# Kernel tuning notes

Measured on AMD Instinct MI355X. Metric: run time of the kernel, lower is better.

## Reference

```python
import jax, jax.numpy as jnp
import numpy as np

N = 50000
E = 800000
D_IN = 64
D_E = 32
H = 128
EPS = 1e-5


def _seg_mean(msgs, dst, n):
    s = jax.ops.segment_sum(msgs, dst, num_segments=n)
    c = jax.ops.segment_sum(jnp.ones((dst.shape[0], 1), msgs.dtype), dst, num_segments=n)
    return s / jnp.maximum(c, 1.0)


def _bn(h, g, b, m, v):
    return g * (h - m) * jax.lax.rsqrt(v + EPS) + b


def setup_inputs() -> dict:
    key = jax.random.key(0)
    ks = jax.random.split(key, 32)
    inp = {
        "x": jax.random.normal(ks[0], (N, D_IN), jnp.float32),
        "edge_index_0": jax.random.randint(ks[1], (2, E), 0, N),
        "edge_index_1": jax.random.randint(ks[2], (2, E), 0, N),
        "edge_index_2": jax.random.randint(ks[3], (2, E), 0, N),
        "edge_attr_0": jax.random.normal(ks[4], (E, D_E), jnp.float32),
        # conv1: Linear(D_IN + D_E -> H)
        "W1": jax.random.normal(ks[5], (H, D_IN + D_E), jnp.float32) * 0.1,
        "b1": jnp.zeros((H,), jnp.float32),
        "g1": jnp.ones((H,), jnp.float32), "be1": jnp.zeros((H,), jnp.float32),
        "m1": jax.random.normal(ks[6], (H,), jnp.float32) * 0.1,
        "v1": jax.random.uniform(ks[7], (H,), jnp.float32) + 0.5,
        # SAGEConv2: lin_l (bias) on aggregated neighbors + lin_r (no bias) on self
        "Wl2": jax.random.normal(ks[8], (H, H), jnp.float32) * 0.1,
        "bl2": jnp.zeros((H,), jnp.float32),
        "Wr2": jax.random.normal(ks[9], (H, H), jnp.float32) * 0.1,
        "g2": jnp.ones((H,), jnp.float32), "be2": jnp.zeros((H,), jnp.float32),
        "m2": jax.random.normal(ks[10], (H,), jnp.float32) * 0.1,
        "v2": jax.random.uniform(ks[11], (H,), jnp.float32) + 0.5,
        # SAGEConv3
        "Wl3": jax.random.normal(ks[12], (H, H), jnp.float32) * 0.1,
        "bl3": jnp.zeros((H,), jnp.float32),
        "Wr3": jax.random.normal(ks[13], (H, H), jnp.float32) * 0.1,
        "g3": jnp.ones((H,), jnp.float32), "be3": jnp.zeros((H,), jnp.float32),
        "m3": jax.random.normal(ks[14], (H,), jnp.float32) * 0.1,
        "v3": jax.random.uniform(ks[15], (H,), jnp.float32) + 0.5,
        # mlp: Linear(H + D_IN -> 64) -> ReLU -> Linear(64 -> 1)
        "W4": jax.random.normal(ks[16], (64, H + D_IN), jnp.float32) * 0.1,
        "b4": jnp.zeros((64,), jnp.float32),
        "W5": jax.random.normal(ks[17], (1, 64), jnp.float32) * 0.1,
        "b5": jnp.zeros((1,), jnp.float32),
    }
    return inp


def reference(x, edge_index_0, edge_index_1, edge_index_2, edge_attr_0,
              W1, b1, g1, be1, m1, v1,
              Wl2, bl2, Wr2, g2, be2, m2, v2,
              Wl3, bl3, Wr3, g3, be3, m3, v3,
              W4, b4, W5, b5):
    n = x.shape[0]
    init = x
    # conv1: gather x_j + edge_attr, concat, linear, mean scatter, relu (update)
    msg = jnp.concatenate([x[edge_index_0[0]], edge_attr_0], axis=-1) @ W1.T + b1  # [E,H]
    h = jax.nn.relu(_seg_mean(msg, edge_index_0[1], n))
    h = jax.nn.relu(_bn(h, g1, be1, m1, v1))  # dropout: eval (identity)
    # conv2: SAGEConv = lin_l(mean_j x_j) + lin_r(x)
    agg = _seg_mean(h[edge_index_1[0]], edge_index_1[1], n)
    h = agg @ Wl2.T + bl2 + h @ Wr2.T
    h = jax.nn.relu(_bn(h, g2, be2, m2, v2))
    # conv3
    agg = _seg_mean(h[edge_index_2[0]], edge_index_2[1], n)
    h = agg @ Wl3.T + bl3 + h @ Wr3.T
    h = jax.nn.relu(_bn(h, g3, be3, m3, v3))
    # readout mlp on [h, initial_embedding]
    z = jnp.concatenate([h, init], axis=1)
    z = jax.nn.relu(z @ W4.T + b4)
    out = (z @ W5.T + b5).squeeze(-1)  # [N]
    return out
```

## Files before the change

kernel.cpp:

```cpp
#include <hip/hip_runtime.h>
#include <hip/hip_bf16.h>
#include <stdint.h>

#define NN 50000
#define NE 800000
#define EPS 1e-5f

#define KB 196
#define SH 8
#define NPB 256
#define RCAP 4500
#define PTP 512
#define PT2 2048

typedef __attribute__((ext_vector_type(8))) short bf16x8;
typedef __attribute__((ext_vector_type(4))) float floatx4;

static __device__ __forceinline__ float bf2f(unsigned int u){
  union { unsigned int i; float f; } c; c.i = u << 16; return c.f;
}
static __device__ __forceinline__ unsigned short f2bf(float f){
  union { float f; unsigned int i; } c; c.f = f;
  unsigned int x = c.i;
  return (unsigned short)((x + 0x7fffu + ((x >> 16) & 1u)) >> 16);
}

#define CVT_X   3200000
#define CVT_W1  3212288
#define CVT_WL2 3228672
#define CVT_WR2 3245056
#define CVT_WL3 3261440
#define CVT_WR3 3277824
#define CVT_END 3290112
__global__ void k_cvt_all(const float* __restrict__ x,  const float* __restrict__ W1,
                          const float* __restrict__ Wl2, const float* __restrict__ Wr2,
                          const float* __restrict__ Wl3, const float* __restrict__ Wr3,
                          const float* __restrict__ W4,
                          unsigned short* __restrict__ xb,  unsigned short* __restrict__ W1b,
                          unsigned short* __restrict__ Wl2b, unsigned short* __restrict__ Wr2b,
                          unsigned short* __restrict__ Wl3b, unsigned short* __restrict__ Wr3b,
                          unsigned short* __restrict__ W4b, int* __restrict__ gcur){
  int i = blockIdx.x * 256 + threadIdx.x;
  if(i >= CVT_END) return;
  if(i < 3 * KB) gcur[i] = 0;
  if(i < CVT_X)        xb[i] = f2bf(x[i]);
  else if(i < CVT_W1)  W1b[i - CVT_X]    = f2bf(W1[i - CVT_X]);
  else if(i < CVT_WL2) Wl2b[i - CVT_W1]  = f2bf(Wl2[i - CVT_W1]);
  else if(i < CVT_WR2) Wr2b[i - CVT_WL2] = f2bf(Wr2[i - CVT_WL2]);
  else if(i < CVT_WL3) Wl3b[i - CVT_WR2] = f2bf(Wl3[i - CVT_WR2]);
  else if(i < CVT_WR3) Wr3b[i - CVT_WL3] = f2bf(Wr3[i - CVT_WL3]);
  else                 W4b[i - CVT_WR3]  = f2bf(W4[i - CVT_WR3]);
}

__global__ void k_partP(const int* __restrict__ ei, const float* __restrict__ ea,
                        int* __restrict__ gcur,
                        int2* __restrict__ recDS, unsigned int* __restrict__ recEA){
  __shared__ int2 stage[PTP];
  __shared__ int slotArr[PTP];
  __shared__ unsigned int pay[PTP * 16];
  __shared__ int hist[KB], ex[KB], cur[KB], gbase[KB];
  __shared__ int tot;
  int tid = threadIdx.x;
  int tile = blockIdx.x * PTP;
  int cnt_local = NE - tile; if(cnt_local > PTP) cnt_local = PTP;
  for(int i = tid; i < KB; i += 256) hist[i] = 0;
  __syncthreads();
  int dst[2], src[2];
  #pragma unroll
  for(int j = 0; j < 2; j++){
    int t = j * 256 + tid;
    if(t < cnt_local){ src[j] = ei[tile + t]; dst[j] = ei[NE + tile + t]; atomicAdd(&hist[dst[j] >> SH], 1); }
    else dst[j] = -1;
  }
  __syncthreads();
  if(tid == 0){ int run = 0; for(int b = 0; b < KB; b++){ ex[b] = run; cur[b] = run; run += hist[b]; } tot = run; }
  if(tid < KB) gbase[tid] = atomicAdd(&gcur[tid], hist[tid]);
  __syncthreads();
  #pragma unroll
  for(int j = 0; j < 2; j++){
    if(dst[j] >= 0){
      int b = dst[j] >> SH;
      int s = atomicAdd(&cur[b], 1);
      stage[s] = make_int2(dst[j], src[j]);
      slotArr[j * 256 + tid] = s;
    }
  }
  __syncthreads();
  {
    int g = tid >> 4, li = tid & 15;
    for(int t = g; t < cnt_local; t += 16){
      int s = slotArr[t];
      float2 v = *(const float2*)(ea + (size_t)(tile + t) * 32 + li * 2);
      pay[s * 16 + li] = (unsigned int)f2bf(v.x) | ((unsigned int)f2bf(v.y) << 16);
    }
  }
  __syncthreads();
  for(int s = tid; s < tot; s += 256){
    int2 r = stage[s];
    int b = r.x >> SH;
    recDS[b * RCAP + gbase[b] + (s - ex[b])] = r;
  }
  {
    int g4 = tid >> 2, l4 = tid & 3;
    for(int s = g4; s < tot; s += 64){
      int b = stage[s].x >> SH;
      int dslot = b * RCAP + gbase[b] + (s - ex[b]);
      uint4 v = *(uint4*)&pay[s * 16 + l4 * 4];
      *((uint4*)(recEA + (size_t)dslot * 16) + l4) = v;
    }
  }
}

__global__ void k_part(const int* __restrict__ ei, int* __restrict__ gcur, int2* __restrict__ rec){
  __shared__ int2 stage[PT2];
  __shared__ int hist[KB], ex[KB], cur[KB], gbase[KB];
  __shared__ int tot;
  int tid = threadIdx.x;
  int tile = blockIdx.x * PT2;
  for(int i = tid; i < KB; i += 256) hist[i] = 0;
  __syncthreads();
  int dst[8], src[8];
  #pragma unroll
  for(int j = 0; j < 8; j++){
    int e = tile + j * 256 + tid;
    if(e < NE){ src[j] = ei[e]; dst[j] = ei[NE + e]; atomicAdd(&hist[dst[j] >> SH], 1); }
    else dst[j] = -1;
  }
  __syncthreads();
  if(tid == 0){ int run = 0; for(int b = 0; b < KB; b++){ ex[b] = run; cur[b] = run; run += hist[b]; } tot = run; }
  if(tid < KB) gbase[tid] = atomicAdd(&gcur[tid], hist[tid]);
  __syncthreads();
  #pragma unroll
  for(int j = 0; j < 8; j++){
    if(dst[j] >= 0){
      int b = dst[j] >> SH;
      int s = atomicAdd(&cur[b], 1);
      stage[s] = make_int2(dst[j], src[j]);
    }
  }
  __syncthreads();
  for(int s = tid; s < tot; s += 256){
    int2 r = stage[s];
    int b = r.x >> SH;
    rec[b * RCAP + gbase[b] + (s - ex[b])] = r;
  }
}

__global__ void k_build0(const int2* __restrict__ rec, const int* __restrict__ gcnt,
                         int2* __restrict__ adj2, int* __restrict__ rowbeg, int* __restrict__ deg){
  __shared__ int cnt[NPB], cur2[NPB];
  __shared__ int part[256];
  int b = blockIdx.x, tid = threadIdx.x;
  int n0 = b << SH;
  int nr = gcnt[b];
  const int2* r = rec + b * RCAP;
  cnt[tid] = 0;
  __syncthreads();
  for(int k = tid; k < nr; k += 256) atomicAdd(&cnt[r[k].x - n0], 1);
  __syncthreads();
  int c0 = cnt[tid];
  part[tid] = c0;
  __syncthreads();
  for(int d = 1; d < 256; d <<= 1){
    int v = (tid >= d) ? part[tid - d] : 0;
    __syncthreads();
    part[tid] += v;
    __syncthreads();
  }
  int base = part[tid] - c0;
  cur2[tid] = base;
  __syncthreads();
  int n = n0 + tid;
  if(n < NN){ rowbeg[n] = b * RCAP + base; deg[n] = c0; }
  for(int k = tid; k < nr; k += 256){
    int2 q = r[k];
    int p = atomicAdd(&cur2[q.x - n0], 1);
    adj2[b * RCAP + p] = make_int2(q.y, b * RCAP + k);
  }
}

__global__ void k_build(const int2* __restrict__ rec, const int* __restrict__ gcnt,
                        int* __restrict__ adj, int* __restrict__ rowbeg, int* __restrict__ deg){
  __shared__ int cnt[NPB], cur2[NPB];
  __shared__ int part[256];
  int b = blockIdx.x, tid = threadIdx.x;
  int n0 = b << SH;
  int nr = gcnt[b];
  const int2* r = rec + b * RCAP;
  cnt[tid] = 0;
  __syncthreads();
  for(int k = tid; k < nr; k += 256) atomicAdd(&cnt[r[k].x - n0], 1);
  __syncthreads();
  int c0 = cnt[tid];
  part[tid] = c0;
  __syncthreads();
  for(int d = 1; d < 256; d <<= 1){
    int v = (tid >= d) ? part[tid - d] : 0;
    __syncthreads();
    part[tid] += v;
    __syncthreads();
  }
  int base = part[tid] - c0;
  cur2[tid] = base;
  __syncthreads();
  int n = n0 + tid;
  if(n < NN){ rowbeg[n] = b * RCAP + base; deg[n] = c0; }
  for(int k = tid; k < nr; k += 256){
    int2 q = r[k];
    int p = atomicAdd(&cur2[q.x - n0], 1);
    adj[b * RCAP + p] = q.y;
  }
}

__global__ void k_aggXE(const int* __restrict__ rowbeg, const int* __restrict__ deg,
                        const int2* __restrict__ adj2,
                        const unsigned short* __restrict__ xb, const unsigned int* __restrict__ recEA,
                        unsigned short* __restrict__ agg){
  int w = (blockIdx.x * blockDim.x + threadIdx.x) >> 6;
  int lane = threadIdx.x & 63;
  if(w >= NN) return;
  int sub = lane >> 4, li = lane & 15;
  int r0 = rowbeg[w], dg = deg[w], r1 = r0 + dg;
  float acc[8] = {0.f,0.f,0.f,0.f,0.f,0.f,0.f,0.f};
  for(int k = r0; k < r1; k += 8){
    int e0 = k + sub, e1 = k + 4 + sub;
    int i0 = e0 < r1 ? e0 : r1 - 1;
    int i1 = e1 < r1 ? e1 : r1 - 1;
    float m0 = e0 < r1 ? 1.f : 0.f;
    float m1 = e1 < r1 ? 1.f : 0.f;
    int2 a0 = adj2[i0], a1 = adj2[i1];
    if(li < 8){
      uint4 v0 = *(const uint4*)(xb + (size_t)a0.x * 64 + li * 8);
      uint4 v1 = *(const uint4*)(xb + (size_t)a1.x * 64 + li * 8);
      acc[0] += m0 * bf2f(v0.x & 0xffffu); acc[1] += m0 * bf2f(v0.x >> 16);
      acc[2] += m0 * bf2f(v0.y & 0xffffu); acc[3] += m0 * bf2f(v0.y >> 16);
      acc[4] += m0 * bf2f(v0.z & 0xffffu); acc[5] += m0 * bf2f(v0.z >> 16);
      acc[6] += m0 * bf2f(v0.w & 0xffffu); acc[7] += m0 * bf2f(v0.w >> 16);
      acc[0] += m1 * bf2f(v1.x & 0xffffu); acc[1] += m1 * bf2f(v1.x >> 16);
      acc[2] += m1 * bf2f(v1.y & 0xffffu); acc[3] += m1 * bf2f(v1.y >> 16);
      acc[4] += m1 * bf2f(v1.z & 0xffffu); acc[5] += m1 * bf2f(v1.z >> 16);
      acc[6] += m1 * bf2f(v1.w & 0xffffu); acc[7] += m1 * bf2f(v1.w >> 16);
    } else {
      int j = li - 8;
      uint2 p0 = *(const uint2*)(recEA + (size_t)a0.y * 16 + j * 2);
      uint2 p1 = *(const uint2*)(recEA + (size_t)a1.y * 16 + j * 2);
      acc[0] += m0 * bf2f(p0.x & 0xffffu); acc[1] += m0 * bf2f(p0.x >> 16);
      acc[2] += m0 * bf2f(p0.y & 0xffffu); acc[3] += m0 * bf2f(p0.y >> 16);
      acc[0] += m1 * bf2f(p1.x & 0xffffu); acc[1] += m1 * bf2f(p1.x >> 16);
      acc[2] += m1 * bf2f(p1.y & 0xffffu); acc[3] += m1 * bf2f(p1.y >> 16);
    }
  }
  #pragma unroll
  for(int d = 16; d < 64; d <<= 1){
    #pragma unroll
    for(int i = 0; i < 8; i++) acc[i] += __shfl_xor(acc[i], d, 64);
  }
  if(sub == 0){
    float inv = 1.0f / (float)(dg > 0 ? dg : 1);
    if(li < 8){
      unsigned int q0 = (unsigned int)f2bf(acc[0]*inv) | ((unsigned int)f2bf(acc[1]*inv) << 16);
      unsigned int q1 = (unsigned int)f2bf(acc[2]*inv) | ((unsigned int)f2bf(acc[3]*inv) << 16);
      unsigned int q2 = (unsigned int)f2bf(acc[4]*inv) | ((unsigned int)f2bf(acc[5]*inv) << 16);
      unsigned int q3 = (unsigned int)f2bf(acc[6]*inv) | ((unsigned int)f2bf(acc[7]*inv) << 16);
      *(uint4*)(agg + (size_t)w * 96 + li * 8) = make_uint4(q0, q1, q2, q3);
    } else {
      int j = li - 8;
      unsigned int q0 = (unsigned int)f2bf(acc[0]*inv) | ((unsigned int)f2bf(acc[1]*inv) << 16);
      unsigned int q1 = (unsigned int)f2bf(acc[2]*inv) | ((unsigned int)f2bf(acc[3]*inv) << 16);
      *(uint2*)(agg + (size_t)w * 96 + 64 + j * 4) = make_uint2(q0, q1);
    }
  }
}

__global__ void k_aggH(const int* __restrict__ rowbeg, const int* __restrict__ deg,
                       const int* __restrict__ adj,
                       const unsigned short* __restrict__ h, unsigned short* __restrict__ agg){
  int w = (blockIdx.x * blockDim.x + threadIdx.x) >> 6;
  int lane = threadIdx.x & 63;
  if(w >= NN) return;
  int sub = lane >> 4, li = lane & 15;
  int r0 = rowbeg[w], dg = deg[w], r1 = r0 + dg;
  float acc[8] = {0.f,0.f,0.f,0.f,0.f,0.f,0.f,0.f};
  for(int k = r0; k < r1; k += 8){
    int e0 = k + sub, e1 = k + 4 + sub;
    int i0 = e0 < r1 ? e0 : r1 - 1;
    int i1 = e1 < r1 ? e1 : r1 - 1;
    float m0 = e0 < r1 ? 1.f : 0.f;
    float m1 = e1 < r1 ? 1.f : 0.f;
    int s0 = adj[i0], s1 = adj[i1];
    uint4 v0 = *(const uint4*)(h + (size_t)s0 * 128 + li * 8);
    uint4 v1 = *(const uint4*)(h + (size_t)s1 * 128 + li * 8);
    acc[0] += m0 * bf2f(v0.x & 0xffffu); acc[1] += m0 * bf2f(v0.x >> 16);
    acc[2] += m0 * bf2f(v0.y & 0xffffu); acc[3] += m0 * bf2f(v0.y >> 16);
    acc[4] += m0 * bf2f(v0.z & 0xffffu); acc[5] += m0 * bf2f(v0.z >> 16);
    acc[6] += m0 * bf2f(v0.w & 0xffffu); acc[7] += m0 * bf2f(v0.w >> 16);
    acc[0] += m1 * bf2f(v1.x & 0xffffu); acc[1] += m1 * bf2f(v1.x >> 16);
    acc[2] += m1 * bf2f(v1.y & 0xffffu); acc[3] += m1 * bf2f(v1.y >> 16);
    acc[4] += m1 * bf2f(v1.z & 0xffffu); acc[5] += m1 * bf2f(v1.z >> 16);
    acc[6] += m1 * bf2f(v1.w & 0xffffu); acc[7] += m1 * bf2f(v1.w >> 16);
  }
  #pragma unroll
  for(int d = 16; d < 64; d <<= 1){
    #pragma unroll
    for(int i = 0; i < 8; i++) acc[i] += __shfl_xor(acc[i], d, 64);
  }
  if(sub == 0){
    float inv = 1.0f / (float)(dg > 0 ? dg : 1);
    unsigned int p0 = (unsigned int)f2bf(acc[0]*inv) | ((unsigned int)f2bf(acc[1]*inv) << 16);
    unsigned int p1 = (unsigned int)f2bf(acc[2]*inv) | ((unsigned int)f2bf(acc[3]*inv) << 16);
    unsigned int p2 = (unsigned int)f2bf(acc[4]*inv) | ((unsigned int)f2bf(acc[5]*inv) << 16);
    unsigned int p3 = (unsigned int)f2bf(acc[6]*inv) | ((unsigned int)f2bf(acc[7]*inv) << 16);
    *(uint4*)(agg + (size_t)w * 128 + li * 8) = make_uint4(p0, p1, p2, p3);
  }
}

__global__ void k_lin1(const unsigned short* __restrict__ agg, const unsigned short* __restrict__ W1,
                       const float* __restrict__ b1,
                       const float* __restrict__ g1, const float* __restrict__ be1,
                       const float* __restrict__ m1, const float* __restrict__ v1,
                       const int* __restrict__ deg, unsigned short* __restrict__ h1){
  int wave = (blockIdx.x * blockDim.x + threadIdx.x) >> 6;
  int lane = threadIdx.x & 63;
  int mt = wave >> 3, nt = wave & 7;
  if(mt >= 3125) return;
  int node0 = mt * 16;
  int col = lane & 15, quad = lane >> 4;
  int o = nt * 16 + col;
  int arow = node0 + col;
  floatx4 acc = {0.f, 0.f, 0.f, 0.f};
  #pragma unroll
  for(int kc = 0; kc < 3; kc++){
    bf16x8 a = *(const bf16x8*)(agg + arow * 96 + kc * 32 + quad * 8);
    bf16x8 b = *(const bf16x8*)(W1 + o * 96 + kc * 32 + quad * 8);
    acc = __builtin_amdgcn_mfma_f32_16x16x32_bf16(a, b, acc, 0, 0, 0);
  }
  float bb = b1[o];
  float sc = g1[o] * rsqrtf(v1[o] + EPS);
  float mv = m1[o], bev = be1[o];
  #pragma unroll
  for(int r = 0; r < 4; r++){
    int node = node0 + quad * 4 + r;
    float pre = (deg[node] > 0) ? (acc[r] + bb) : 0.0f;
    float t = fmaxf(pre, 0.f);
    float bn = sc * (t - mv) + bev;
    h1[node * 128 + o] = f2bf(fmaxf(bn, 0.f));
  }
}

__global__ void k_sage(const unsigned short* __restrict__ agg, const unsigned short* __restrict__ hin,
                       const unsigned short* __restrict__ Wl, const float* __restrict__ bl,
                       const unsigned short* __restrict__ Wr,
                       const float* __restrict__ g, const float* __restrict__ be,
                       const float* __restrict__ m, const float* __restrict__ v,
                       unsigned short* __restrict__ hout){
  int wave = (blockIdx.x * blockDim.x + threadIdx.x) >> 6;
  int lane = threadIdx.x & 63;
  int mt = wave >> 3, nt = wave & 7;
  if(mt >= 3125) return;
  int node0 = mt * 16;
  int col = lane & 15, quad = lane >> 4;
  int o = nt * 16 + col;
  int arow = node0 + col;
  floatx4 acc = {0.f, 0.f, 0.f, 0.f};
  #pragma unroll
  for(int kc = 0; kc < 4; kc++){
    bf16x8 a = *(const bf16x8*)(agg + arow * 128 + kc * 32 + quad * 8);
    bf16x8 b = *(const bf16x8*)(Wl + o * 128 + kc * 32 + quad * 8);
    acc = __builtin_amdgcn_mfma_f32_16x16x32_bf16(a, b, acc, 0, 0, 0);
  }
  #pragma unroll
  for(int kc = 0; kc < 4; kc++){
    bf16x8 a = *(const bf16x8*)(hin + arow * 128 + kc * 32 + quad * 8);
    bf16x8 b = *(const bf16x8*)(Wr + o * 128 + kc * 32 + quad * 8);
    acc = __builtin_amdgcn_mfma_f32_16x16x32_bf16(a, b, acc, 0, 0, 0);
  }
  float blv = bl[o];
  float sc = g[o] * rsqrtf(v[o] + EPS);
  float mv = m[o], bev = be[o];
  #pragma unroll
  for(int r = 0; r < 4; r++){
    int node = node0 + quad * 4 + r;
    float pre = acc[r] + blv;
    float bn = sc * (pre - mv) + bev;
    hout[node * 128 + o] = f2bf(fmaxf(bn, 0.f));
  }
}

__global__ void k_readout(const unsigned short* __restrict__ h3, const unsigned short* __restrict__ xb,
                          const unsigned short* __restrict__ W4, const float* __restrict__ b4,
                          const float* __restrict__ W5, const float* __restrict__ b5,
                          float* __restrict__ out){
  int wave = (blockIdx.x * blockDim.x + threadIdx.x) >> 6;
  int lane = threadIdx.x & 63;
  if(wave >= 3125) return;
  int node0 = wave * 16;
  int col = lane & 15, quad = lane >> 4;
  int arow = node0 + col;
  float partial[4] = {0.f, 0.f, 0.f, 0.f};
  #pragma unroll
  for(int nt = 0; nt < 4; nt++){
    int o = nt * 16 + col;
    floatx4 acc = {0.f, 0.f, 0.f, 0.f};
    #pragma unroll
    for(int kc = 0; kc < 4; kc++){
      bf16x8 a = *(const bf16x8*)(h3 + arow * 128 + kc * 32 + quad * 8);
      bf16x8 b = *(const bf16x8*)(W4 + o * 192 + kc * 32 + quad * 8);
      acc = __builtin_amdgcn_mfma_f32_16x16x32_bf16(a, b, acc, 0, 0, 0);
    }
    #pragma unroll
    for(int kc = 0; kc < 2; kc++){
      bf16x8 a = *(const bf16x8*)(xb + arow * 64 + kc * 32 + quad * 8);
      bf16x8 b = *(const bf16x8*)(W4 + o * 192 + 128 + kc * 32 + quad * 8);
      acc = __builtin_amdgcn_mfma_f32_16x16x32_bf16(a, b, acc, 0, 0, 0);
    }
    float bb = b4[o];
    float w5 = W5[o];
    #pragma unroll
    for(int r = 0; r < 4; r++)
      partial[r] += fmaxf(acc[r] + bb, 0.f) * w5;
  }
  #pragma unroll
  for(int d = 1; d < 16; d <<= 1){
    #pragma unroll
    for(int r = 0; r < 4; r++)
      partial[r] += __shfl_xor(partial[r], d, 64);
  }
  if(col == 0){
    float b5f = b5[0];
    #pragma unroll
    for(int r = 0; r < 4; r++)
      out[node0 + quad * 4 + r] = partial[r] + b5f;
  }
}

extern "C" void kernel_launch(void* const* d_in, const int* in_sizes, int n_in,
                              void* d_out, int out_size, void* d_ws, size_t ws_size,
                              hipStream_t stream) {
  const float* x   = (const float*)d_in[0];
  const int* ei0   = (const int*)d_in[1];
  const int* ei1   = (const int*)d_in[2];
  const int* ei2   = (const int*)d_in[3];
  const float* ea  = (const float*)d_in[4];
  const float* W1  = (const float*)d_in[5];
  const float* b1  = (const float*)d_in[6];
  const float* g1  = (const float*)d_in[7];
  const float* be1 = (const float*)d_in[8];
  const float* m1  = (const float*)d_in[9];
  const float* v1  = (const float*)d_in[10];
  const float* Wl2 = (const float*)d_in[11];
  const float* bl2 = (const float*)d_in[12];
  const float* Wr2 = (const float*)d_in[13];
  const float* g2  = (const float*)d_in[14];
  const float* be2 = (const float*)d_in[15];
  const float* m2  = (const float*)d_in[16];
  const float* v2  = (const float*)d_in[17];
  const float* Wl3 = (const float*)d_in[18];
  const float* bl3 = (const float*)d_in[19];
  const float* Wr3 = (const float*)d_in[20];
  const float* g3  = (const float*)d_in[21];
  const float* be3 = (const float*)d_in[22];
  const float* m3  = (const float*)d_in[23];
  const float* v3  = (const float*)d_in[24];
  const float* W4  = (const float*)d_in[25];
  const float* b4  = (const float*)d_in[26];
  const float* W5  = (const float*)d_in[27];
  const float* b5  = (const float*)d_in[28];

  char* ws = (char*)d_ws;
  size_t off = 0;
  auto alloc = [&](size_t bytes) -> void* {
    void* p = (void*)(ws + off);
    off += (bytes + 255) & ~(size_t)255;
    return p;
  };
  int* gcur    = (int*)alloc(3 * KB * sizeof(int));
  int* rowbeg3 = (int*)alloc(3 * NN * sizeof(int));
  int* deg3    = (int*)alloc(3 * NN * sizeof(int));
  int2* recDS  = (int2*)alloc((size_t)KB * RCAP * 8);
  int2* adj2   = (int2*)alloc((size_t)KB * RCAP * 8);
  unsigned int* recEA = (unsigned int*)alloc((size_t)KB * RCAP * 64);
  unsigned short* agg1 = (unsigned short*)alloc((size_t)NN * 96 * 2);
  unsigned short* xb   = (unsigned short*)alloc((size_t)NN * 64 * 2);
  unsigned short* W1b  = (unsigned short*)alloc(12288 * 2);
  unsigned short* Wl2b = (unsigned short*)alloc(16384 * 2);
  unsigned short* Wr2b = (unsigned short*)alloc(16384 * 2);
  unsigned short* Wl3b = (unsigned short*)alloc(16384 * 2);
  unsigned short* Wr3b = (unsigned short*)alloc(16384 * 2);
  unsigned short* W4b  = (unsigned short*)alloc(12288 * 2);

  int* adjI = (int*)adj2;

  unsigned short* h1   = (unsigned short*)recEA;
  unsigned short* aggH = h1 + (size_t)NN * 128;
  unsigned short* h2   = h1 + (size_t)2 * NN * 128;
  unsigned short* h3   = h1 + (size_t)3 * NN * 128;

  int* rb0 = rowbeg3;            int* dg0 = deg3;
  int* rb1 = rowbeg3 + NN;       int* dg1 = deg3 + NN;
  int* rb2 = rowbeg3 + 2 * NN;   int* dg2 = deg3 + 2 * NN;

  const int gPP   = (NE + PTP - 1) / PTP;
  const int gP2   = (NE + PT2 - 1) / PT2;
  const int gAgg  = (NN * 64) / 256;
  const int gTile = (3125 * 8 * 64) / 256;
  const int gRead = (3125 * 64 + 255) / 256;
  const int gCvt  = (CVT_END + 255) / 256;

  k_cvt_all<<<gCvt, 256, 0, stream>>>(x, W1, Wl2, Wr2, Wl3, Wr3, W4,
                                      xb, W1b, Wl2b, Wr2b, Wl3b, Wr3b, W4b, gcur);

  k_partP<<<gPP, 256, 0, stream>>>(ei0, ea, gcur, recDS, recEA);
  k_build0<<<KB, 256, 0, stream>>>(recDS, gcur, adj2, rb0, dg0);
  k_aggXE<<<gAgg, 256, 0, stream>>>(rb0, dg0, adj2, xb, recEA, agg1);
  k_lin1<<<gTile, 256, 0, stream>>>(agg1, W1b, b1, g1, be1, m1, v1, dg0, h1);

  k_part<<<gP2, 256, 0, stream>>>(ei1, gcur + KB, recDS);
  k_build<<<KB, 256, 0, stream>>>(recDS, gcur + KB, adjI, rb1, dg1);
  k_aggH<<<gAgg, 256, 0, stream>>>(rb1, dg1, adjI, h1, aggH);
  k_sage<<<gTile, 256, 0, stream>>>(aggH, h1, Wl2b, bl2, Wr2b, g2, be2, m2, v2, h2);

  k_part<<<gP2, 256, 0, stream>>>(ei2, gcur + 2 * KB, recDS);
  k_build<<<KB, 256, 0, stream>>>(recDS, gcur + 2 * KB, adjI, rb2, dg2);
  k_aggH<<<gAgg, 256, 0, stream>>>(rb2, dg2, adjI, h2, aggH);
  k_sage<<<gTile, 256, 0, stream>>>(aggH, h2, Wl3b, bl3, Wr3b, g3, be3, m3, v3, h3);

  k_readout<<<gRead, 256, 0, stream>>>(h3, xb, W4b, b4, W5, b5, (float*)d_out);

  (void)in_sizes; (void)n_in; (void)out_size; (void)ws_size;
}
```

Measured before the change: 565.9 us.

## Parallelize bucket prefix scan and scatter edge-attr payload directly to global

Replaces the single-thread serial exclusive scan over the 196 destination buckets with a parallel Hillis-Steele scan in both partition kernels. In the edge-attribute partition kernel, the shared-memory staging buffer for the bf16 payload is removed and each edge's absolute destination slot is computed up front, so the payload is written straight to its bucketed position. The tile size is doubled to 1024 edges per block. This cuts serial work and shared memory traffic, but the payload writes to global become scattered 4-byte stores instead of coalesced 16-byte stores.

```diff
diff --git a/kernel.cpp b/kernel.cpp
--- a/kernel.cpp
+++ b/kernel.cpp
@@ -10,7 +10,7 @@
 #define SH 8
 #define NPB 256
 #define RCAP 4500
-#define PTP 512
+#define PTP 1024
 #define PT2 2048
 
 typedef __attribute__((ext_vector_type(8))) short bf16x8;
@@ -56,42 +56,47 @@
                         int* __restrict__ gcur,
                         int2* __restrict__ recDS, unsigned int* __restrict__ recEA){
   __shared__ int2 stage[PTP];
-  __shared__ int slotArr[PTP];
-  __shared__ unsigned int pay[PTP * 16];
+  __shared__ int slotAbs[PTP];
   __shared__ int hist[KB], ex[KB], cur[KB], gbase[KB];
+  __shared__ int part[256];
   __shared__ int tot;
   int tid = threadIdx.x;
   int tile = blockIdx.x * PTP;
   int cnt_local = NE - tile; if(cnt_local > PTP) cnt_local = PTP;
   for(int i = tid; i < KB; i += 256) hist[i] = 0;
   __syncthreads();
-  int dst[2], src[2];
-  #pragma unroll
-  for(int j = 0; j < 2; j++){
+  int dst[4], src[4];
+  #pragma unroll
+  for(int j = 0; j < 4; j++){
     int t = j * 256 + tid;
     if(t < cnt_local){ src[j] = ei[tile + t]; dst[j] = ei[NE + tile + t]; atomicAdd(&hist[dst[j] >> SH], 1); }
     else dst[j] = -1;
   }
   __syncthreads();
-  if(tid == 0){ int run = 0; for(int b = 0; b < KB; b++){ ex[b] = run; cur[b] = run; run += hist[b]; } tot = run; }
-  if(tid < KB) gbase[tid] = atomicAdd(&gcur[tid], hist[tid]);
-  __syncthreads();
-  #pragma unroll
-  for(int j = 0; j < 2; j++){
+  int c0 = (tid < KB) ? hist[tid] : 0;
+  part[tid] = c0;
+  __syncthreads();
+  for(int d = 1; d < 256; d <<= 1){
+    int v = (tid >= d) ? part[tid - d] : 0;
+    __syncthreads();
+    part[tid] += v;
+    __syncthreads();
+  }
+  if(tid < KB){
+    int e = part[tid] - c0;
+    ex[tid] = e; cur[tid] = e;
+    gbase[tid] = atomicAdd(&gcur[tid], c0);
+  }
+  if(tid == 255) tot = part[255];
+  __syncthreads();
+  #pragma unroll
+  for(int j = 0; j < 4; j++){
+    int t = j * 256 + tid;
     if(dst[j] >= 0){
       int b = dst[j] >> SH;
       int s = atomicAdd(&cur[b], 1);
       stage[s] = make_int2(dst[j], src[j]);
-      slotArr[j * 256 + tid] = s;
-    }
-  }
-  __syncthreads();
-  {
-    int g = tid >> 4, li = tid & 15;
-    for(int t = g; t < cnt_local; t += 16){
-      int s = slotArr[t];
-      float2 v = *(const float2*)(ea + (size_t)(tile + t) * 32 + li * 2);
-      pay[s * 16 + li] = (unsigned int)f2bf(v.x) | ((unsigned int)f2bf(v.y) << 16);
+      slotAbs[t] = b * RCAP + gbase[b] + (s - ex[b]);
     }
   }
   __syncthreads();
@@ -101,12 +106,11 @@
     recDS[b * RCAP + gbase[b] + (s - ex[b])] = r;
   }
   {
-    int g4 = tid >> 2, l4 = tid & 3;
-    for(int s = g4; s < tot; s += 64){
-      int b = stage[s].x >> SH;
-      int dslot = b * RCAP + gbase[b] + (s - ex[b]);
-      uint4 v = *(uint4*)&pay[s * 16 + l4 * 4];
-      *((uint4*)(recEA + (size_t)dslot * 16) + l4) = v;
+    int g = tid >> 4, li = tid & 15;
+    for(int t = g; t < cnt_local; t += 16){
+      int ds = slotAbs[t];
+      float2 v = *(const float2*)(ea + (size_t)(tile + t) * 32 + li * 2);
+      recEA[(size_t)ds * 16 + li] = (unsigned int)f2bf(v.x) | ((unsigned int)f2bf(v.y) << 16);
     }
   }
 }
@@ -114,6 +118,7 @@
 __global__ void k_part(const int* __restrict__ ei, int* __restrict__ gcur, int2* __restrict__ rec){
   __shared__ int2 stage[PT2];
   __shared__ int hist[KB], ex[KB], cur[KB], gbase[KB];
+  __shared__ int part[256];
   __shared__ int tot;
   int tid = threadIdx.x;
   int tile = blockIdx.x * PT2;
@@ -127,8 +132,21 @@
     else dst[j] = -1;
   }
   __syncthreads();
-  if(tid == 0){ int run = 0; for(int b = 0; b < KB; b++){ ex[b] = run; cur[b] = run; run += hist[b]; } tot = run; }
-  if(tid < KB) gbase[tid] = atomicAdd(&gcur[tid], hist[tid]);
+  int c0 = (tid < KB) ? hist[tid] : 0;
+  part[tid] = c0;
+  __syncthreads();
+  for(int d = 1; d < 256; d <<= 1){
+    int v = (tid >= d) ? part[tid - d] : 0;
+    __syncthreads();
+    part[tid] += v;
+    __syncthreads();
+  }
+  if(tid < KB){
+    int e = part[tid] - c0;
+    ex[tid] = e; cur[tid] = e;
+    gbase[tid] = atomicAdd(&gcur[tid], c0);
+  }
+  if(tid == 255) tot = part[255];
   __syncthreads();
   #pragma unroll
   for(int j = 0; j < 8; j++){
```

Measured after the change: 567.8 us. Within noise of the previous version (+0.3%).
